# Kernel optimization log

Hardware: AMD Instinct MI355X
Metric: run time of the kernel (lower is better)

Reference implementation:

```python
import jax, jax.numpy as jnp
import numpy as np

N, D, G, C, M = 4096, 256, 4, 10, 5  # nodes, feat dim, batches, centroids, clusterings


def setup_inputs() -> dict:
    key = jax.random.key(0)
    k1, k2, k3, k4 = jax.random.split(key, 4)
    adj = jax.random.uniform(k1, (N, N), dtype=jnp.float32)
    enc_rep = jax.random.normal(k2, (N, D), dtype=jnp.float32)
    batch_id = jax.random.randint(k3, (N,), 0, G, dtype=jnp.int32)
    cluster_labels = jax.random.randint(k4, (M, N), 0, C, dtype=jnp.int32)
    return {"adj": adj, "enc_rep": enc_rep, "batch_id": batch_id,
            "cluster_labels": cluster_labels, "top_k": 20, "top_k_inter": 10}


def reference(adj, enc_rep, batch_id, cluster_labels, top_k, top_k_inter):
    n = enc_rep.shape[0]
    NEG = jnp.float32(-1e30)
    rows = jnp.arange(n)

    # 'similarity' metric: raw inner-product similarity, full N x N once
    sim = enc_rep @ enc_rep.T                                # [N, N]
    same = batch_id[:, None] == batch_id[None, :]            # same-batch mask

    # intra: top_k+1 within own batch group, drop first (self) column
    intra_sim = jnp.where(same, sim, NEG)
    _, intra_idx = jax.lax.top_k(intra_sim, top_k + 1)
    intra_idx = intra_idx[:, 1:]                              # [N, top_k]

    # inter: top_k_inter among all other batch groups
    inter_sim = jnp.where(same, NEG, sim)
    _, inter_idx = jax.lax.top_k(inter_sim, top_k_inter)      # [N, top_k_inter]

    knn_idx = jnp.concatenate([intra_idx, inter_idx], axis=1)  # [N, k_tot]

    # rep_adj[j, i] = 1 iff j is a knn of i  (coo rows=neighbors, cols=node)
    B = jnp.zeros((n, n), jnp.float32).at[knn_idx, rows[:, None]].set(1.0)
    # common_adj = rep_adj * (rep_adj.T > 0), diag zeroed (mutual-knn graph)
    common = B * B.T
    common = common.at[rows, rows].set(0.0)

    # locality = knn_neighbor * adj
    locality = common * adj

    # padded-neighbor validity mask (I_knn_padded != -1 analog): mutual neighbors
    mutual = common[rows[:, None], knn_idx] > 0               # [N, k_tot]

    # per-clustering close-neighbor test, combined across clusterings
    nb_lbl = cluster_labels[:, knn_idx]                       # [M, N, k_tot]
    eq = cluster_labels[:, :, None] == nb_lbl                 # [M, N, k_tot]
    curr = eq | mutual[None]                                  # curr_close_nei = eq | bool_mask
    all_close = jnp.all(curr, axis=0)                         # AND across clusterings

    return locality, all_close.astype(jnp.float32)
```

## Files before the change

### kernel.cpp

```cpp
#include <hip/hip_runtime.h>
#include <hip/hip_bf16.h>
#include <cfloat>

#define NN 4096
#define DD 256
#define MM 5
#define GG 4
#define K_TOT 30
#define TGT_INTRA 32
#define TGT_INTER 24
#define CAND_CAP 64

typedef __attribute__((ext_vector_type(8))) short bf16x8;
typedef __attribute__((ext_vector_type(4))) float f32x4;

__device__ __forceinline__ void async16(const void* g, void* l) {
    __builtin_amdgcn_global_load_lds((__attribute__((address_space(1))) void*)g,
                                     (__attribute__((address_space(3))) void*)l,
                                     16, 0, 0);
}

__global__ __launch_bounds__(256) void convert_bf16(const float* __restrict__ E,
                                                    ushort* __restrict__ Eb) {
    const int idx = blockIdx.x * 256 + threadIdx.x;
    const float4 f = ((const float4*)E)[idx];
    ushort4 h;
    {
        __hip_bfloat16 a = __float2bfloat16(f.x); h.x = *(ushort*)&a;
        __hip_bfloat16 b = __float2bfloat16(f.y); h.y = *(ushort*)&b;
        __hip_bfloat16 c = __float2bfloat16(f.z); h.z = *(ushort*)&c;
        __hip_bfloat16 d = __float2bfloat16(f.w); h.w = *(ushort*)&d;
    }
    ((ushort4*)Eb)[idx] = h;
}

__global__ __launch_bounds__(256) void build_mask(const int* __restrict__ batch,
                                                  unsigned long long* __restrict__ maskTab) {
    const int j = blockIdx.x * 256 + threadIdx.x;
    const int b = batch[j];
    const int wv = j >> 6;
#pragma unroll
    for (int g = 0; g < GG; ++g) {
        const unsigned long long m = __ballot(b != g);
        if ((threadIdx.x & 63) == 0) maskTab[g * (NN / 64) + wv] = m;
    }
}

__global__ __launch_bounds__(256) void gemm_bf16(const ushort* __restrict__ Eb,
                                                 ushort* __restrict__ simb) {
    __shared__ union {
        struct { ushort A[128 * 32]; ushort B[128 * 32]; } s;
        ushort stage[32 * 136];
    } lds;

    const int t = threadIdx.x;
    const int w = t >> 6, lane = t & 63;
    const int quad = lane >> 4, mr = lane & 15;
    const int rowBase = blockIdx.y * 128, colBase = blockIdx.x * 128;
    const int waveRow = (w & 1) * 64, waveCol = (w >> 1) * 64;

    const int lrow = lane >> 2;
    const int lslot = lane & 3;
    const int gchunk = lslot ^ ((lrow >> 1) & 3);

    f32x4 acc[4][4];
#pragma unroll
    for (int a = 0; a < 4; ++a)
#pragma unroll
        for (int b = 0; b < 4; ++b) acc[a][b] = (f32x4)(0.0f);

    for (int kc = 0; kc < DD; kc += 32) {
#pragma unroll
        for (int n = 0; n < 2; ++n) {
            const int r = w * 32 + n * 16 + lrow;
            const ushort* ga = Eb + (size_t)(rowBase + r) * DD + kc + gchunk * 8;
            const ushort* gb = Eb + (size_t)(colBase + r) * DD + kc + gchunk * 8;
            async16(ga, &lds.s.A[(w * 32 + n * 16) * 32]);
            async16(gb, &lds.s.B[(w * 32 + n * 16) * 32]);
        }
        __syncthreads();

        const int swzF = (mr >> 1) & 3;
        bf16x8 af[4], bfr[4];
#pragma unroll
        for (int rt = 0; rt < 4; ++rt)
            af[rt] = *(const bf16x8*)&lds.s.A[(waveRow + rt * 16 + mr) * 32 +
                                              ((quad ^ swzF) * 8)];
#pragma unroll
        for (int ct = 0; ct < 4; ++ct)
            bfr[ct] = *(const bf16x8*)&lds.s.B[(waveCol + ct * 16 + mr) * 32 +
                                               ((quad ^ swzF) * 8)];
#pragma unroll
        for (int rt = 0; rt < 4; ++rt)
#pragma unroll
            for (int ct = 0; ct < 4; ++ct)
                acc[rt][ct] = __builtin_amdgcn_mfma_f32_16x16x32_bf16(
                    af[rt], bfr[ct], acc[rt][ct], 0, 0, 0);
        __syncthreads();
    }

#pragma unroll
    for (int c = 0; c < 4; ++c) {
        __syncthreads();
        if ((w & 1) == (c >> 1)) {
            const int rtBase = 2 * (c & 1);
#pragma unroll
            for (int r2 = 0; r2 < 2; ++r2) {
                const int rt = rtBase + r2;
#pragma unroll
                for (int ct = 0; ct < 4; ++ct)
#pragma unroll
                    for (int reg = 0; reg < 4; ++reg) {
                        __hip_bfloat16 hb = __float2bfloat16(acc[rt][ct][reg]);
                        const int lr2 = r2 * 16 + quad * 4 + reg;
                        lds.stage[lr2 * 136 + waveCol + ct * 16 + mr] = *(ushort*)&hb;
                    }
            }
        }
        __syncthreads();
#pragma unroll
        for (int it = 0; it < 2; ++it) {
            const int cid = t + it * 256;
            const int row = cid >> 4;
            const int off = (cid & 15) * 8;
            *(int4*)(simb + (size_t)(rowBase + c * 32 + row) * NN + colBase + off) =
                *(const int4*)&lds.stage[row * 136 + off];
        }
    }
}

__global__ __launch_bounds__(128, 8) void select_rescore(
        const ushort* __restrict__ sim,
        const float* __restrict__ E,
        const int* __restrict__ batch,
        const unsigned long long* __restrict__ maskTab,
        int* __restrict__ knn) {
    __shared__ unsigned histS[256];
    __shared__ unsigned subS[256];
    __shared__ int candIdxS[2][CAND_CAP];
    __shared__ double candValS[2][CAND_CAP];
    __shared__ int cntS[2];
    __shared__ int cbS[2];
    __shared__ unsigned remS[2];
    __shared__ unsigned thrS[2];

    const int t = threadIdx.x;
    const int w = t >> 6, lane = t & 63;
    const int i = blockIdx.x;
    const int bi = batch[i];

    histS[t] = 0u; histS[t + 128] = 0u;
    subS[t] = 0u;  subS[t + 128] = 0u;
    if (t < 2) cntS[t] = 0;
    __syncthreads();

    unsigned kp[16];
    unsigned interm = 0;
    {
        const ushort* sp = sim + (size_t)i * NN + t * 8;
        const unsigned long long* mp = maskTab + bi * (NN / 64) + (t >> 3);
        const int sh = (t & 7) * 8;
#pragma unroll
        for (int c = 0; c < 4; ++c) {
            const int4 sv = *(const int4*)(sp + c * 1024);
            const unsigned mb = (unsigned)(mp[c * 16] >> sh) & 0xFFu;
            interm |= mb << (c * 8);
            const unsigned uu[4] = {(unsigned)sv.x, (unsigned)sv.y,
                                    (unsigned)sv.z, (unsigned)sv.w};
#pragma unroll
            for (int p = 0; p < 4; ++p) {
                const unsigned u = uu[p];
                const unsigned sgn = u & 0x80008000u;
                const unsigned k2 = u ^ (0x80008000u | ((sgn >> 15) * 0x7FFFu));
                kp[c * 4 + p] = k2;
                const unsigned m0 = (mb >> (2 * p)) & 1u;
                const unsigned m1 = (mb >> (2 * p + 1)) & 1u;
                atomicAdd(&histS[(k2 >> 8) & 0xFF], m0 ? 0x10000u : 1u);
                atomicAdd(&histS[k2 >> 24], m1 ? 0x10000u : 1u);
            }
        }
    }
    __syncthreads();

    {
        const unsigned* hb = &histS[lane * 4];
        const unsigned s4 = hb[0] + hb[1] + hb[2] + hb[3];
        unsigned suf = s4;
#pragma unroll
        for (int off = 1; off < 64; off <<= 1) {
            const unsigned o = __shfl_down(suf, off);
            if (lane + off < 64) suf += o;
        }
        unsigned cum = suf - s4;
#pragma unroll
        for (int b = 3; b >= 0; --b) {
            const unsigned h = hb[b];
            const unsigned prev = cum;
            cum += h;
            if ((cum & 0xFFFFu) >= TGT_INTRA && (prev & 0xFFFFu) < TGT_INTRA) {
                cbS[0] = lane * 4 + b;
                remS[0] = TGT_INTRA - (prev & 0xFFFFu);
            }
            if ((cum >> 16) >= TGT_INTER && (prev >> 16) < TGT_INTER) {
                cbS[1] = lane * 4 + b;
                remS[1] = TGT_INTER - (prev >> 16);
            }
        }
    }
    __syncthreads();

    {
        const int cb0 = cbS[0], cb1 = cbS[1];
#pragma unroll
        for (int c = 0; c < 4; ++c)
#pragma unroll
            for (int p = 0; p < 4; ++p) {
                const unsigned k2 = kp[c * 4 + p];
                const unsigned k0 = k2 & 0xFFFFu, k1 = k2 >> 16;
                const int m0 = (interm >> (c * 8 + 2 * p)) & 1;
                const int m1 = (interm >> (c * 8 + 2 * p + 1)) & 1;
                if ((int)(k0 >> 8) == (m0 ? cb1 : cb0))
                    atomicAdd(&subS[k0 & 0xFF], m0 ? 0x10000u : 1u);
                if ((int)(k1 >> 8) == (m1 ? cb1 : cb0))
                    atomicAdd(&subS[k1 & 0xFF], m1 ? 0x10000u : 1u);
            }
    }
    __syncthreads();

    {
        const unsigned rI = remS[0], rT = remS[1];
        const int cb0 = cbS[0], cb1 = cbS[1];
        const unsigned* sb = &subS[lane * 4];
        const unsigned s4 = sb[0] + sb[1] + sb[2] + sb[3];
        unsigned suf = s4;
#pragma unroll
        for (int off = 1; off < 64; off <<= 1) {
            const unsigned o = __shfl_down(suf, off);
            if (lane + off < 64) suf += o;
        }
        unsigned cum = suf - s4;
#pragma unroll
        for (int b = 3; b >= 0; --b) {
            const unsigned h = sb[b];
            const unsigned prev = cum;
            cum += h;
            if ((cum & 0xFFFFu) >= rI && (prev & 0xFFFFu) < rI)
                thrS[0] = ((unsigned)cb0 << 8) | (unsigned)(lane * 4 + b);
            if ((cum >> 16) >= rT && (prev >> 16) < rT)
                thrS[1] = ((unsigned)cb1 << 8) | (unsigned)(lane * 4 + b);
        }
    }
    __syncthreads();

    {
        const unsigned thr0 = thrS[0], thr1 = thrS[1];
#pragma unroll
        for (int c = 0; c < 4; ++c)
#pragma unroll
            for (int p = 0; p < 4; ++p) {
                const unsigned k2 = kp[c * 4 + p];
                const unsigned k0 = k2 & 0xFFFFu, k1 = k2 >> 16;
                const int m0 = (interm >> (c * 8 + 2 * p)) & 1;
                const int m1 = (interm >> (c * 8 + 2 * p + 1)) & 1;
                if (k0 >= (m0 ? thr1 : thr0)) {
                    const int pos = atomicAdd(&cntS[m0], 1);
                    if (pos < CAND_CAP) candIdxS[m0][pos] = c * 1024 + t * 8 + 2 * p;
                }
                if (k1 >= (m1 ? thr1 : thr0)) {
                    const int pos = atomicAdd(&cntS[m1], 1);
                    if (pos < CAND_CAP) candIdxS[m1][pos] = c * 1024 + t * 8 + 2 * p + 1;
                }
            }
    }
    __syncthreads();

    const int c0 = min(cntS[0], CAND_CAP);
    const int c1 = min(cntS[1], CAND_CAP);
    {
        const int tot = c0 + c1;
        const float* ei = E + (size_t)i * DD;
        if (t < tot) {
            const int m = (t < c0) ? 0 : 1;
            const int s = m ? (t - c0) : t;
            const int j = candIdxS[m][s];
            const float* ej = E + (size_t)j * DD;
            double a0 = 0, a1 = 0, a2 = 0, a3 = 0;
#pragma unroll 8
            for (int k = 0; k < DD; k += 4) {
                const float4 e = *(const float4*)(ej + k);
                a0 = fma((double)ei[k + 0], (double)e.x, a0);
                a1 = fma((double)ei[k + 1], (double)e.y, a1);
                a2 = fma((double)ei[k + 2], (double)e.z, a2);
                a3 = fma((double)ei[k + 3], (double)e.w, a3);
            }
            candValS[m][s] = (a0 + a1) + (a2 + a3);
        }
    }
    __syncthreads();

    if (w == 0) {
        if (lane < c0) {
            const double v = candValS[0][lane];
            const int idx = candIdxS[0][lane];
            int r = 0;
            for (int s = 0; s < c0; ++s) {
                const double o = candValS[0][s];
                const int oi = candIdxS[0][s];
                r += (o > v) || (o == v && oi < idx);
            }
            if (r >= 1 && r <= 20) knn[i * K_TOT + r - 1] = idx;
        }
    } else {
        if (lane < c1) {
            const double v = candValS[1][lane];
            const int idx = candIdxS[1][lane];
            int r = 0;
            for (int s = 0; s < c1; ++s) {
                const double o = candValS[1][s];
                const int oi = candIdxS[1][s];
                r += (o > v) || (o == v && oi < idx);
            }
            if (r < 10) knn[i * K_TOT + 20 + r] = idx;
        }
    }
}

__global__ __launch_bounds__(256) void finalize_k(const int* __restrict__ knn,
                                                  const float* __restrict__ adj,
                                                  const int* __restrict__ cl,
                                                  float* __restrict__ out) {
    const int gid = blockIdx.x * 256 + threadIdx.x;
    if (gid >= NN * K_TOT) return;
    const int i = gid / K_TOT;
    const int j = knn[gid];

    bool mutual = false;
#pragma unroll
    for (int s = 0; s < K_TOT; ++s) mutual |= (knn[j * K_TOT + s] == i);

    if (mutual) out[(size_t)i * NN + j] = adj[(size_t)i * NN + j];

    bool ac = mutual;
    if (!ac) {
        bool alleq = true;
#pragma unroll
        for (int m = 0; m < MM; ++m) alleq &= (cl[m * NN + i] == cl[m * NN + j]);
        ac = alleq;
    }
    out[(size_t)NN * NN + gid] = ac ? 1.0f : 0.0f;
}

extern "C" void kernel_launch(void* const* d_in, const int* in_sizes, int n_in,
                              void* d_out, int out_size, void* d_ws, size_t ws_size,
                              hipStream_t stream) {
    const float* adj = (const float*)d_in[0];
    const float* enc = (const float*)d_in[1];
    const int* batch = (const int*)d_in[2];
    const int* cl = (const int*)d_in[3];
    float* out = (float*)d_out;

    const size_t simB = (size_t)NN * NN * sizeof(ushort);
    const size_t ebB = (size_t)NN * DD * sizeof(ushort);
    const size_t knnB = (size_t)NN * K_TOT * sizeof(int);
    const size_t maskB = (size_t)GG * (NN / 64) * sizeof(unsigned long long);

    const dim3 gGrid(NN / 128, NN / 128);

    if (ws_size >= simB + ebB + knnB + maskB) {
        ushort* simb = (ushort*)d_ws;
        ushort* Eb = (ushort*)((char*)d_ws + simB);
        int* knn = (int*)((char*)d_ws + simB + ebB);
        unsigned long long* maskTab =
            (unsigned long long*)((char*)d_ws + simB + ebB + knnB);
        hipMemsetAsync(d_out, 0, (size_t)NN * NN * sizeof(float), stream);
        convert_bf16<<<NN * DD / 4 / 256, 256, 0, stream>>>(enc, Eb);
        build_mask<<<NN / 256, 256, 0, stream>>>(batch, maskTab);
        gemm_bf16<<<gGrid, 256, 0, stream>>>(Eb, simb);
        select_rescore<<<NN, 128, 0, stream>>>(simb, enc, batch, maskTab, knn);
        finalize_k<<<(NN * K_TOT + 255) / 256, 256, 0, stream>>>(knn, adj, cl, out);
    } else {
        ushort* simb = (ushort*)d_out;
        ushort* Eb = (ushort*)d_ws;
        int* knn = (int*)((char*)d_ws + ebB);
        unsigned long long* maskTab =
            (unsigned long long*)((char*)d_ws + ebB + knnB);
        convert_bf16<<<NN * DD / 4 / 256, 256, 0, stream>>>(enc, Eb);
        build_mask<<<NN / 256, 256, 0, stream>>>(batch, maskTab);
        gemm_bf16<<<gGrid, 256, 0, stream>>>(Eb, simb);
        select_rescore<<<NN, 128, 0, stream>>>(simb, enc, batch, maskTab, knn);
        hipMemsetAsync(d_out, 0, (size_t)NN * NN * sizeof(float), stream);
        finalize_k<<<(NN * K_TOT + 255) / 256, 256, 0, stream>>>(knn, adj, cl, out);
    }
}
```

Baseline: 203.6 us.

## Double-buffer GEMM loads, replicate histogram bins, split rescore, fuse prep kernels

Several changes at once. The GEMM now prefetches the next K-chunk into a second LDS buffer while computing the current one, so there is one barrier per step. The select kernel loads its sim and mask values up front, spreads histogram atomics over 4 replicated bins per bucket to cut LDS contention, and splits each candidate's fp64 dot product across 4 lanes with a shuffle reduction. The bf16 conversion and mask-build kernels are merged into one launch. In exchange the GEMM uses more LDS and the histogram needs an extra merge pass.

```diff
diff --git a/kernel.cpp b/kernel.cpp
--- a/kernel.cpp
+++ b/kernel.cpp
@@ -20,9 +20,11 @@
                                      16, 0, 0);
 }
 
-__global__ __launch_bounds__(256) void convert_bf16(const float* __restrict__ E,
-                                                    ushort* __restrict__ Eb) {
-    const int idx = blockIdx.x * 256 + threadIdx.x;
+__global__ __launch_bounds__(256) void convert_and_mask(
+        const float* __restrict__ E, ushort* __restrict__ Eb,
+        const int* __restrict__ batch, unsigned long long* __restrict__ maskTab) {
+    const int t = threadIdx.x;
+    const int idx = blockIdx.x * 256 + t;
     const float4 f = ((const float4*)E)[idx];
     ushort4 h;
     {
@@ -32,24 +34,26 @@
         __hip_bfloat16 d = __float2bfloat16(f.w); h.w = *(ushort*)&d;
     }
     ((ushort4*)Eb)[idx] = h;
-}
-
-__global__ __launch_bounds__(256) void build_mask(const int* __restrict__ batch,
-                                                  unsigned long long* __restrict__ maskTab) {
-    const int j = blockIdx.x * 256 + threadIdx.x;
-    const int b = batch[j];
-    const int wv = j >> 6;
-#pragma unroll
-    for (int g = 0; g < GG; ++g) {
-        const unsigned long long m = __ballot(b != g);
-        if ((threadIdx.x & 63) == 0) maskTab[g * (NN / 64) + wv] = m;
+
+    if (blockIdx.x == 0) {
+#pragma unroll
+        for (int wv = 0; wv < NN / 256; ++wv) {
+            const int j = wv * 256 + t;
+            const int b = batch[j];
+#pragma unroll
+            for (int g = 0; g < GG; ++g) {
+                const unsigned long long m = __ballot(b != g);
+                if ((t & 63) == 0)
+                    maskTab[g * (NN / 64) + wv * 4 + (t >> 6)] = m;
+            }
+        }
     }
 }
 
 __global__ __launch_bounds__(256) void gemm_bf16(const ushort* __restrict__ Eb,
                                                  ushort* __restrict__ simb) {
     __shared__ union {
-        struct { ushort A[128 * 32]; ushort B[128 * 32]; } s;
+        struct { ushort A[2][128 * 32]; ushort B[2][128 * 32]; } s;
         ushort stage[32 * 136];
     } lds;
 
@@ -63,33 +67,43 @@
     const int lslot = lane & 3;
     const int gchunk = lslot ^ ((lrow >> 1) & 3);
 
+    const ushort* gA0 = Eb + (size_t)(rowBase + w * 32 + 0 + lrow) * DD + gchunk * 8;
+    const ushort* gA1 = Eb + (size_t)(rowBase + w * 32 + 16 + lrow) * DD + gchunk * 8;
+    const ushort* gB0 = Eb + (size_t)(colBase + w * 32 + 0 + lrow) * DD + gchunk * 8;
+    const ushort* gB1 = Eb + (size_t)(colBase + w * 32 + 16 + lrow) * DD + gchunk * 8;
+
     f32x4 acc[4][4];
 #pragma unroll
     for (int a = 0; a < 4; ++a)
 #pragma unroll
         for (int b = 0; b < 4; ++b) acc[a][b] = (f32x4)(0.0f);
 
-    for (int kc = 0; kc < DD; kc += 32) {
-#pragma unroll
-        for (int n = 0; n < 2; ++n) {
-            const int r = w * 32 + n * 16 + lrow;
-            const ushort* ga = Eb + (size_t)(rowBase + r) * DD + kc + gchunk * 8;
-            const ushort* gb = Eb + (size_t)(colBase + r) * DD + kc + gchunk * 8;
-            async16(ga, &lds.s.A[(w * 32 + n * 16) * 32]);
-            async16(gb, &lds.s.B[(w * 32 + n * 16) * 32]);
-        }
-        __syncthreads();
+    async16(gA0, &lds.s.A[0][(w * 32 + 0) * 32]);
+    async16(gA1, &lds.s.A[0][(w * 32 + 16) * 32]);
+    async16(gB0, &lds.s.B[0][(w * 32 + 0) * 32]);
+    async16(gB1, &lds.s.B[0][(w * 32 + 16) * 32]);
+    __syncthreads();
+
+    for (int kt = 0; kt < 8; ++kt) {
+        const int cur = kt & 1;
+        if (kt < 7) {
+            const int kc = (kt + 1) * 32;
+            async16(gA0 + kc, &lds.s.A[cur ^ 1][(w * 32 + 0) * 32]);
+            async16(gA1 + kc, &lds.s.A[cur ^ 1][(w * 32 + 16) * 32]);
+            async16(gB0 + kc, &lds.s.B[cur ^ 1][(w * 32 + 0) * 32]);
+            async16(gB1 + kc, &lds.s.B[cur ^ 1][(w * 32 + 16) * 32]);
+        }
 
         const int swzF = (mr >> 1) & 3;
         bf16x8 af[4], bfr[4];
 #pragma unroll
         for (int rt = 0; rt < 4; ++rt)
-            af[rt] = *(const bf16x8*)&lds.s.A[(waveRow + rt * 16 + mr) * 32 +
-                                              ((quad ^ swzF) * 8)];
+            af[rt] = *(const bf16x8*)&lds.s.A[cur][(waveRow + rt * 16 + mr) * 32 +
+                                                   ((quad ^ swzF) * 8)];
 #pragma unroll
         for (int ct = 0; ct < 4; ++ct)
-            bfr[ct] = *(const bf16x8*)&lds.s.B[(waveCol + ct * 16 + mr) * 32 +
-                                               ((quad ^ swzF) * 8)];
+            bfr[ct] = *(const bf16x8*)&lds.s.B[cur][(waveCol + ct * 16 + mr) * 32 +
+                                                    ((quad ^ swzF) * 8)];
 #pragma unroll
         for (int rt = 0; rt < 4; ++rt)
 #pragma unroll
@@ -135,7 +149,8 @@
         const int* __restrict__ batch,
         const unsigned long long* __restrict__ maskTab,
         int* __restrict__ knn) {
-    __shared__ unsigned histS[256];
+    __shared__ unsigned histS[1024];
+    __shared__ unsigned mergedS[256];
     __shared__ unsigned subS[256];
     __shared__ int candIdxS[2][CAND_CAP];
     __shared__ double candValS[2][CAND_CAP];
@@ -146,11 +161,13 @@
 
     const int t = threadIdx.x;
     const int w = t >> 6, lane = t & 63;
+    const int rep = lane & 3;
     const int i = blockIdx.x;
     const int bi = batch[i];
 
-    histS[t] = 0u; histS[t + 128] = 0u;
-    subS[t] = 0u;  subS[t + 128] = 0u;
+#pragma unroll
+    for (int z = 0; z < 8; ++z) histS[t + z * 128] = 0u;
+    subS[t] = 0u; subS[t + 128] = 0u;
     if (t < 2) cntS[t] = 0;
     __syncthreads();
 
@@ -160,13 +177,19 @@
         const ushort* sp = sim + (size_t)i * NN + t * 8;
         const unsigned long long* mp = maskTab + bi * (NN / 64) + (t >> 3);
         const int sh = (t & 7) * 8;
+        int4 sv[4];
+        unsigned long long mw[4];
 #pragma unroll
         for (int c = 0; c < 4; ++c) {
-            const int4 sv = *(const int4*)(sp + c * 1024);
-            const unsigned mb = (unsigned)(mp[c * 16] >> sh) & 0xFFu;
+            sv[c] = *(const int4*)(sp + c * 1024);
+            mw[c] = mp[c * 16];
+        }
+#pragma unroll
+        for (int c = 0; c < 4; ++c) {
+            const unsigned mb = (unsigned)(mw[c] >> sh) & 0xFFu;
             interm |= mb << (c * 8);
-            const unsigned uu[4] = {(unsigned)sv.x, (unsigned)sv.y,
-                                    (unsigned)sv.z, (unsigned)sv.w};
+            const unsigned uu[4] = {(unsigned)sv[c].x, (unsigned)sv[c].y,
+                                    (unsigned)sv[c].z, (unsigned)sv[c].w};
 #pragma unroll
             for (int p = 0; p < 4; ++p) {
                 const unsigned u = uu[p];
@@ -175,15 +198,25 @@
                 kp[c * 4 + p] = k2;
                 const unsigned m0 = (mb >> (2 * p)) & 1u;
                 const unsigned m1 = (mb >> (2 * p + 1)) & 1u;
-                atomicAdd(&histS[(k2 >> 8) & 0xFF], m0 ? 0x10000u : 1u);
-                atomicAdd(&histS[k2 >> 24], m1 ? 0x10000u : 1u);
-            }
-        }
-    }
-    __syncthreads();
-
-    {
-        const unsigned* hb = &histS[lane * 4];
+                atomicAdd(&histS[(((k2 >> 8) & 0xFF) << 2) + rep], m0 ? 0x10000u : 1u);
+                atomicAdd(&histS[((k2 >> 24) << 2) + rep], m1 ? 0x10000u : 1u);
+            }
+        }
+    }
+    __syncthreads();
+
+#pragma unroll
+    for (int k = 0; k < 8; ++k) {
+        const int wd = t + 128 * k;
+        unsigned v = histS[wd];
+        v += __shfl_xor(v, 1);
+        v += __shfl_xor(v, 2);
+        if ((lane & 3) == 0) mergedS[wd >> 2] = v;
+    }
+    __syncthreads();
+
+    {
+        const unsigned* hb = &mergedS[lane * 4];
         const unsigned s4 = hb[0] + hb[1] + hb[2] + hb[3];
         unsigned suf = s4;
 #pragma unroll
@@ -278,22 +311,30 @@
     const int c1 = min(cntS[1], CAND_CAP);
     {
         const int tot = c0 + c1;
-        const float* ei = E + (size_t)i * DD;
-        if (t < tot) {
-            const int m = (t < c0) ? 0 : 1;
-            const int s = m ? (t - c0) : t;
-            const int j = candIdxS[m][s];
-            const float* ej = E + (size_t)j * DD;
-            double a0 = 0, a1 = 0, a2 = 0, a3 = 0;
-#pragma unroll 8
-            for (int k = 0; k < DD; k += 4) {
-                const float4 e = *(const float4*)(ej + k);
-                a0 = fma((double)ei[k + 0], (double)e.x, a0);
-                a1 = fma((double)ei[k + 1], (double)e.y, a1);
-                a2 = fma((double)ei[k + 2], (double)e.z, a2);
-                a3 = fma((double)ei[k + 3], (double)e.w, a3);
-            }
-            candValS[m][s] = (a0 + a1) + (a2 + a3);
+        const int sub = t & 3;
+        const float* eis = E + (size_t)i * DD + sub * 64;
+        for (int base = 0; base < tot; base += 32) {
+            const int slot = base + (t >> 2);
+            if (slot < tot) {
+                const int m = (slot < c0) ? 0 : 1;
+                const int s = m ? (slot - c0) : slot;
+                const int j = candIdxS[m][s];
+                const float* ej = E + (size_t)j * DD + sub * 64;
+                double a0 = 0, a1 = 0, a2 = 0, a3 = 0;
+#pragma unroll
+                for (int k = 0; k < 64; k += 4) {
+                    const float4 e = *(const float4*)(ej + k);
+                    const float4 f = *(const float4*)(eis + k);
+                    a0 = fma((double)f.x, (double)e.x, a0);
+                    a1 = fma((double)f.y, (double)e.y, a1);
+                    a2 = fma((double)f.z, (double)e.z, a2);
+                    a3 = fma((double)f.w, (double)e.w, a3);
+                }
+                double v = (a0 + a1) + (a2 + a3);
+                v += __shfl_xor(v, 1);
+                v += __shfl_xor(v, 2);
+                if (sub == 0) candValS[m][s] = v;
+            }
         }
     }
     __syncthreads();
@@ -373,8 +414,7 @@
         unsigned long long* maskTab =
             (unsigned long long*)((char*)d_ws + simB + ebB + knnB);
         hipMemsetAsync(d_out, 0, (size_t)NN * NN * sizeof(float), stream);
-        convert_bf16<<<NN * DD / 4 / 256, 256, 0, stream>>>(enc, Eb);
-        build_mask<<<NN / 256, 256, 0, stream>>>(batch, maskTab);
+        convert_and_mask<<<NN * DD / 4 / 256, 256, 0, stream>>>(enc, Eb, batch, maskTab);
         gemm_bf16<<<gGrid, 256, 0, stream>>>(Eb, simb);
         select_rescore<<<NN, 128, 0, stream>>>(simb, enc, batch, maskTab, knn);
         finalize_k<<<(NN * K_TOT + 255) / 256, 256, 0, stream>>>(knn, adj, cl, out);
@@ -384,8 +424,7 @@
         int* knn = (int*)((char*)d_ws + ebB);
         unsigned long long* maskTab =
             (unsigned long long*)((char*)d_ws + ebB + knnB);
-        convert_bf16<<<NN * DD / 4 / 256, 256, 0, stream>>>(enc, Eb);
-        build_mask<<<NN / 256, 256, 0, stream>>>(batch, maskTab);
+        convert_and_mask<<<NN * DD / 4 / 256, 256, 0, stream>>>(enc, Eb, batch, maskTab);
         gemm_bf16<<<gGrid, 256, 0, stream>>>(Eb, simb);
         select_rescore<<<NN, 128, 0, stream>>>(simb, enc, batch, maskTab, knn);
         hipMemsetAsync(d_out, 0, (size_t)NN * NN * sizeof(float), stream);
```

After: 229.9 us. 1.13x slower.
